# Optimization experiments

Hardware: AMD Instinct MI355X
Metric: run time of the kernel (lower is better)

The kernel has to match this reference:

```python
import jax, jax.numpy as jnp
import numpy as np

N_GENE = 100000
N_DIS = 20000
H = 128
E = 500000


def setup_inputs() -> dict:
    key = jax.random.key(0)
    ks = jax.random.split(key, 12)
    s1 = 1.0 / np.sqrt(2 * H)  # fan-in init scale, Linear(2H, H)
    s2 = 1.0 / np.sqrt(H)      # fan-in init scale, Linear(H, 1)
    z_gene = jax.random.normal(ks[0], (N_GENE, H), jnp.float32)
    z_disease = jax.random.normal(ks[1], (N_DIS, H), jnp.float32)
    # gene->disease edges: row indexes genes, col indexes diseases
    edges_gd = jnp.stack([
        jax.random.randint(ks[2], (E,), 0, N_GENE),
        jax.random.randint(ks[3], (E,), 0, N_DIS),
    ])
    # gene->gene edges
    edges_gg = jnp.stack([
        jax.random.randint(ks[4], (E,), 0, N_GENE),
        jax.random.randint(ks[5], (E,), 0, N_GENE),
    ])
    return {
        "z_gene": z_gene,
        "z_disease": z_disease,
        "edges_gd": edges_gd,
        "edges_gg": edges_gg,
        "w1_gd": jax.random.normal(ks[6], (2 * H, H), jnp.float32) * s1,
        "b1_gd": jnp.zeros((H,), jnp.float32),
        "w2_gd": jax.random.normal(ks[7], (H, 1), jnp.float32) * s2,
        "b2_gd": jnp.zeros((1,), jnp.float32),
        "w1_gg": jax.random.normal(ks[8], (2 * H, H), jnp.float32) * s1,
        "b1_gg": jnp.zeros((H,), jnp.float32),
        "w2_gg": jax.random.normal(ks[9], (H, 1), jnp.float32) * s2,
        "b2_gg": jnp.zeros((1,), jnp.float32),
    }


def _decode(z_src, z_dst, edges, w1, b1, w2, b2):
    # gather src/dst node embeddings by edge index, concat -> [E, 2H]
    z = jnp.concatenate([z_src[edges[0]], z_dst[edges[1]]], axis=1)
    h = jnp.maximum(z @ w1 + b1, 0.0)  # Linear + ReLU
    return h @ w2 + b2                  # Linear -> [E, 1]


def reference(z_gene, z_disease, edges_gd, edges_gg,
              w1_gd, b1_gd, w2_gd, b2_gd,
              w1_gg, b1_gg, w2_gg, b2_gg):
    out_gd = _decode(z_gene, z_disease, edges_gd, w1_gd, b1_gd, w2_gd, b2_gd)
    out_gg = _decode(z_gene, z_gene, edges_gg, w1_gg, b1_gg, w2_gg, b2_gg)
    # dict of per-relation outputs in the original; stack since E matches
    return jnp.stack([out_gd, out_gg])  # [2, E, 1]
```

## Files before the change

### kernel.cpp

```cpp
#include <hip/hip_runtime.h>
#include <hip/hip_bf16.h>

#define HDIM 128

typedef __attribute__((ext_vector_type(8))) short short8;
typedef __attribute__((ext_vector_type(4))) float floatx4;

__device__ __forceinline__ float bf2f(unsigned short u) {
    return __uint_as_float(((unsigned)u) << 16);
}
__device__ __forceinline__ unsigned short f2b(float f) {
    __hip_bfloat16 h = __float2bfloat16(f);
    return __builtin_bit_cast(unsigned short, h);
}
__device__ __forceinline__ float ldv(const void* p, size_t i, int flag) {
    return flag ? bf2f(((const unsigned short*)p)[i]) : ((const float*)p)[i];
}
__device__ __forceinline__ short8 pack8(float4 a, float4 b) {
    short8 r;
    r[0] = (short)f2b(a.x); r[1] = (short)f2b(a.y);
    r[2] = (short)f2b(a.z); r[3] = (short)f2b(a.w);
    r[4] = (short)f2b(b.x); r[5] = (short)f2b(b.y);
    r[6] = (short)f2b(b.z); r[7] = (short)f2b(b.w);
    return r;
}

__global__ __launch_bounds__(256) void detect_kernel(
    const unsigned short* __restrict__ zbits, int* __restrict__ flag)
{
    __shared__ int red[256];
    int tid = threadIdx.x;
    int cnt = 0;
    for (int i = tid; i < 4096; i += 256) {
        int ex = (zbits[i] >> 7) & 0xFF;
        if (ex >= 100 && ex <= 140) cnt++;
    }
    red[tid] = cnt;
    __syncthreads();
    for (int s = 128; s > 0; s >>= 1) {
        if (tid < s) red[tid] += red[tid + s];
        __syncthreads();
    }
    if (tid == 0) *flag = (red[0] >= 3686) ? 1 : 0;
}

__global__ __launch_bounds__(256) void wprep_kernel(
    const void* __restrict__ w1_gd, const void* __restrict__ w1_gg,
    const void* __restrict__ b1_gd, const void* __restrict__ w2_gd,
    const void* __restrict__ b2_gd, const void* __restrict__ b1_gg,
    const void* __restrict__ w2_gg, const void* __restrict__ b2_gg,
    unsigned short* __restrict__ img, float* __restrict__ params,
    const int* __restrict__ flagp)
{
    int b = blockIdx.x;
    int flag = *flagp;
    if (b < 4) {
        const void* w1 = (b < 2) ? w1_gd : w1_gg;
        int part = b & 1;
        unsigned short* out = img + b * 16384;
        for (int idx = threadIdx.x; idx < 16384; idx += 256) {
            int n   = idx >> 7;
            int rem = idx & 127;
            int g   = (rem >> 3) ^ (n & 15);
            int j   = rem & 7;
            size_t s = (size_t)(part * 128 + g * 8 + j) * 128 + n;
            out[idx] = flag ? ((const unsigned short*)w1)[s]
                            : f2b(((const float*)w1)[s]);
        }
    } else {
        int t = threadIdx.x;
        if (t < 128) {
            params[t]       = ldv(b1_gd, t, flag);
            params[256 + t] = ldv(b1_gg, t, flag);
        } else {
            params[t]       = ldv(w2_gd, t - 128, flag);
            params[256 + t] = ldv(w2_gg, t - 128, flag);
        }
        if (t == 0) {
            params[512] = ldv(b2_gd, 0, flag);
            params[513] = ldv(b2_gg, 0, flag);
        }
    }
}

__device__ __forceinline__ void load_zfrags(
    const void* Z, int r0c, int r1c, int quad, int flag, short8 zf[2][4])
{
    if (flag) {
        const uint4* z0 = (const uint4*)Z + (size_t)r0c * 16;
        const uint4* z1 = (const uint4*)Z + (size_t)r1c * 16;
#pragma unroll
        for (int kc = 0; kc < 4; ++kc) {
            zf[0][kc] = __builtin_bit_cast(short8, z0[kc * 4 + quad]);
            zf[1][kc] = __builtin_bit_cast(short8, z1[kc * 4 + quad]);
        }
    } else {
        const float4* z0 = (const float4*)Z + (size_t)r0c * 32;
        const float4* z1 = (const float4*)Z + (size_t)r1c * 32;
#pragma unroll
        for (int kc = 0; kc < 4; ++kc) {
            int o = kc * 8 + quad * 2;
            zf[0][kc] = pack8(z0[o], z0[o + 1]);
            zf[1][kc] = pack8(z1[o], z1[o + 1]);
        }
    }
}

__device__ __forceinline__ void mfma_pass_store(
    const uint4* sW, const short8 zf[2][4], int nl, int quad,
    int row0, int row1, int M, unsigned short* __restrict__ Out)
{
    floatx4 acc[2][8];
#pragma unroll
    for (int rt = 0; rt < 2; ++rt)
#pragma unroll
        for (int nt = 0; nt < 8; ++nt)
            acc[rt][nt] = (floatx4){0.f, 0.f, 0.f, 0.f};

#pragma unroll
    for (int kc = 0; kc < 4; ++kc) {
        int p = (kc * 4 + quad) ^ nl;
#pragma unroll
        for (int nt = 0; nt < 8; ++nt) {
            short8 wf = __builtin_bit_cast(short8, sW[(nt * 16 + nl) * 16 + p]);
            acc[0][nt] = __builtin_amdgcn_mfma_f32_16x16x32_bf16(wf, zf[0][kc], acc[0][nt], 0, 0, 0);
            acc[1][nt] = __builtin_amdgcn_mfma_f32_16x16x32_bf16(wf, zf[1][kc], acc[1][nt], 0, 0, 0);
        }
    }
#pragma unroll
    for (int rt = 0; rt < 2; ++rt) {
        int row = rt ? row1 : row0;
        if (row < M) {
#pragma unroll
            for (int nt = 0; nt < 8; ++nt) {
                ushort4 v;
                v.x = f2b(acc[rt][nt][0]);
                v.y = f2b(acc[rt][nt][1]);
                v.z = f2b(acc[rt][nt][2]);
                v.w = f2b(acc[rt][nt][3]);
                *(ushort4*)(Out + (size_t)row * HDIM + nt * 16 + quad * 4) = v;
            }
        }
    }
}

__global__ __launch_bounds__(256) void proj_gene3_kernel(
    const void* __restrict__ Z, const uint4* __restrict__ Wimg,
    unsigned short* __restrict__ A_gd, unsigned short* __restrict__ A_gg,
    unsigned short* __restrict__ B_gg, int M, const int* __restrict__ flagp)
{
    __shared__ uint4 sW[2048];
    int tid  = threadIdx.x;
    int lane = tid & 63;
    int wave = tid >> 6;
    int nl   = lane & 15;
    int quad = lane >> 4;

    int row0 = blockIdx.x * 128 + wave * 32 + nl;
    int row1 = row0 + 16;
    int r0c = row0 < M ? row0 : (M - 1);
    int r1c = row1 < M ? row1 : (M - 1);

    short8 zf[2][4];
    load_zfrags(Z, r0c, r1c, quad, *flagp, zf);

    const uint4* imgs[3] = {Wimg, Wimg + 2 * 2048, Wimg + 3 * 2048};
    unsigned short* outs[3] = {A_gd, A_gg, B_gg};
#pragma unroll
    for (int ph = 0; ph < 3; ++ph) {
        __syncthreads();
        const uint4* im = imgs[ph];
#pragma unroll
        for (int i = 0; i < 8; ++i) sW[tid + i * 256] = im[tid + i * 256];
        __syncthreads();
        mfma_pass_store(sW, zf, nl, quad, row0, row1, M, outs[ph]);
    }
}

__global__ __launch_bounds__(256) void proj1_kernel(
    const void* __restrict__ Z, const uint4* __restrict__ Wimg,
    unsigned short* __restrict__ Out, int M, const int* __restrict__ flagp)
{
    __shared__ uint4 sW[2048];
    int tid  = threadIdx.x;
    int lane = tid & 63;
    int wave = tid >> 6;
    int nl   = lane & 15;
    int quad = lane >> 4;

    int row0 = blockIdx.x * 128 + wave * 32 + nl;
    int row1 = row0 + 16;
    int r0c = row0 < M ? row0 : (M - 1);
    int r1c = row1 < M ? row1 : (M - 1);

    short8 zf[2][4];
    load_zfrags(Z, r0c, r1c, quad, *flagp, zf);

#pragma unroll
    for (int i = 0; i < 8; ++i) sW[tid + i * 256] = Wimg[tid + i * 256];
    __syncthreads();
    mfma_pass_store(sW, zf, nl, quad, row0, row1, M, Out);
}

__global__ __launch_bounds__(256) void edge_kernel(
    const int* __restrict__ edges_gd, const int* __restrict__ edges_gg,
    const unsigned short* __restrict__ A_gd, const unsigned short* __restrict__ B_gd,
    const unsigned short* __restrict__ A_gg, const unsigned short* __restrict__ B_gg,
    const float* __restrict__ params,
    void* __restrict__ out, int E, int eblk, const int* __restrict__ flagp)
{
    int rel = (blockIdx.x >= eblk) ? 1 : 0;
    int blk = blockIdx.x - rel * eblk;
    const int* edges = rel ? edges_gg : edges_gd;
    const unsigned short* A = rel ? A_gg : A_gd;
    const unsigned short* B = rel ? B_gg : B_gd;
    const float* pp = params + rel * 256;
    float b2f = params[512 + rel];
    size_t eoff = rel ? (size_t)E : 0;

    int tid  = threadIdx.x;
    int lane = tid & 63;
    int wave = tid >> 6;
    int nl   = lane & 7;
    int grp  = lane >> 3;

    float b1f[16], w2f[16];
#pragma unroll
    for (int i = 0; i < 4; ++i) {
        float4 tb = *(const float4*)(pp + nl * 16 + i * 4);
        float4 tw = *(const float4*)(pp + 128 + nl * 16 + i * 4);
        b1f[i * 4 + 0] = tb.x; b1f[i * 4 + 1] = tb.y;
        b1f[i * 4 + 2] = tb.z; b1f[i * 4 + 3] = tb.w;
        w2f[i * 4 + 0] = tw.x; w2f[i * 4 + 1] = tw.y;
        w2f[i * 4 + 2] = tw.z; w2f[i * 4 + 3] = tw.w;
    }

    int e = blk * 32 + wave * 8 + grp;
    float acc = 0.f;
    if (e < E) {
        int src = edges[e];
        int dst = edges[E + e];
        const uint4* ap = (const uint4*)(A + (size_t)src * HDIM) + nl * 2;
        const uint4* bp = (const uint4*)(B + (size_t)dst * HDIM) + nl * 2;
        uint4 a0 = ap[0], a1 = ap[1];
        uint4 c0 = bp[0], c1 = bp[1];
        const unsigned* au0 = (const unsigned*)&a0;
        const unsigned* au1 = (const unsigned*)&a1;
        const unsigned* cu0 = (const unsigned*)&c0;
        const unsigned* cu1 = (const unsigned*)&c1;
#pragma unroll
        for (int i = 0; i < 4; ++i) {
            float x0 = __uint_as_float(au0[i] << 16);
            float x1 = __uint_as_float(au0[i] & 0xffff0000u);
            float y0 = __uint_as_float(cu0[i] << 16);
            float y1 = __uint_as_float(cu0[i] & 0xffff0000u);
            float h0 = fmaxf(x0 + y0 + b1f[2 * i], 0.f);
            float h1 = fmaxf(x1 + y1 + b1f[2 * i + 1], 0.f);
            acc = fmaf(h0, w2f[2 * i], acc);
            acc = fmaf(h1, w2f[2 * i + 1], acc);
        }
#pragma unroll
        for (int i = 0; i < 4; ++i) {
            float x0 = __uint_as_float(au1[i] << 16);
            float x1 = __uint_as_float(au1[i] & 0xffff0000u);
            float y0 = __uint_as_float(cu1[i] << 16);
            float y1 = __uint_as_float(cu1[i] & 0xffff0000u);
            float h0 = fmaxf(x0 + y0 + b1f[8 + 2 * i], 0.f);
            float h1 = fmaxf(x1 + y1 + b1f[8 + 2 * i + 1], 0.f);
            acc = fmaf(h0, w2f[8 + 2 * i], acc);
            acc = fmaf(h1, w2f[8 + 2 * i + 1], acc);
        }
    }
    acc += __shfl_xor(acc, 1);
    acc += __shfl_xor(acc, 2);
    acc += __shfl_xor(acc, 4);
    if (e < E && nl == 0) {
        float r = acc + b2f;
        if (*flagp) ((unsigned short*)out)[eoff + e] = f2b(r);
        else        ((float*)out)[eoff + e] = r;
    }
}

__global__ __launch_bounds__(128) void naive_edge_kernel(
    const int* __restrict__ edges,
    const void* __restrict__ zsrc, const void* __restrict__ zdst,
    const void* __restrict__ w1, const void* __restrict__ b1,
    const void* __restrict__ w2, const void* __restrict__ b2,
    void* __restrict__ out, size_t eoff, int E,
    const int* __restrict__ flagp)
{
    int flag = flagp ? *flagp : 0;
    __shared__ float zs[128], zd[128], red[128];
    int e = blockIdx.x;
    int n = threadIdx.x;
    int src = edges[e], dst = edges[E + e];
    zs[n] = ldv(zsrc, (size_t)src * HDIM + n, flag);
    zd[n] = ldv(zdst, (size_t)dst * HDIM + n, flag);
    __syncthreads();
    float acc = ldv(b1, n, flag);
    for (int k = 0; k < 128; ++k) acc = fmaf(zs[k], ldv(w1, (size_t)k * HDIM + n, flag), acc);
    for (int k = 0; k < 128; ++k) acc = fmaf(zd[k], ldv(w1, (size_t)(128 + k) * HDIM + n, flag), acc);
    red[n] = fmaxf(acc, 0.f) * ldv(w2, n, flag);
    __syncthreads();
    for (int s = 64; s > 0; s >>= 1) {
        if (n < s) red[n] += red[n + s];
        __syncthreads();
    }
    if (n == 0) {
        float r = red[0] + ldv(b2, 0, flag);
        if (flag) ((unsigned short*)out)[eoff + e] = f2b(r);
        else      ((float*)out)[eoff + e] = r;
    }
}

extern "C" void kernel_launch(void* const* d_in, const int* in_sizes, int n_in,
                              void* d_out, int out_size, void* d_ws, size_t ws_size,
                              hipStream_t stream)
{
    const void* z_gene = d_in[0];
    const void* z_dis  = d_in[1];
    const int* edges_gd = (const int*)d_in[2];
    const int* edges_gg = (const int*)d_in[3];
    const void* w1_gd = d_in[4];
    const void* b1_gd = d_in[5];
    const void* w2_gd = d_in[6];
    const void* b2_gd = d_in[7];
    const void* w1_gg = d_in[8];
    const void* b1_gg = d_in[9];
    const void* w2_gg = d_in[10];
    const void* b2_gg = d_in[11];

    int NG = in_sizes[0] / HDIM;
    int ND = in_sizes[1] / HDIM;
    int E  = in_sizes[2] / 2;

    size_t off_flag   = 0;
    size_t off_params = 256;
    size_t off_img    = 2560;
    size_t off_Agd    = off_img + 131072;
    size_t off_Bgd    = off_Agd + (size_t)NG * HDIM * 2;
    size_t off_Agg    = off_Bgd + (size_t)ND * HDIM * 2;
    size_t off_Bgg    = off_Agg + (size_t)NG * HDIM * 2;
    size_t need       = off_Bgg + (size_t)NG * HDIM * 2;

    char* ws = (char*)d_ws;

    if (ws_size < need) {
        const int* flagp = nullptr;
        if (ws_size >= 16) {
            detect_kernel<<<1, 256, 0, stream>>>((const unsigned short*)z_gene, (int*)ws);
            flagp = (const int*)ws;
        }
        naive_edge_kernel<<<E, 128, 0, stream>>>(edges_gd, z_gene, z_dis,
                                                 w1_gd, b1_gd, w2_gd, b2_gd,
                                                 d_out, 0, E, flagp);
        naive_edge_kernel<<<E, 128, 0, stream>>>(edges_gg, z_gene, z_gene,
                                                 w1_gg, b1_gg, w2_gg, b2_gg,
                                                 d_out, (size_t)E, E, flagp);
        return;
    }

    int* flag = (int*)(ws + off_flag);
    float* params = (float*)(ws + off_params);
    unsigned short* img = (unsigned short*)(ws + off_img);
    unsigned short* Agd = (unsigned short*)(ws + off_Agd);
    unsigned short* Bgd = (unsigned short*)(ws + off_Bgd);
    unsigned short* Agg = (unsigned short*)(ws + off_Agg);
    unsigned short* Bgg = (unsigned short*)(ws + off_Bgg);

    detect_kernel<<<1, 256, 0, stream>>>((const unsigned short*)z_gene, flag);

    wprep_kernel<<<5, 256, 0, stream>>>(w1_gd, w1_gg, b1_gd, w2_gd, b2_gd,
                                        b1_gg, w2_gg, b2_gg, img, params, flag);

    const uint4* img4 = (const uint4*)img;
    int gblk = (NG + 127) / 128;
    int dblk = (ND + 127) / 128;
    proj_gene3_kernel<<<gblk, 256, 0, stream>>>(z_gene, img4, Agd, Agg, Bgg, NG, flag);
    proj1_kernel<<<dblk, 256, 0, stream>>>(z_dis, img4 + 2048, Bgd, ND, flag);

    int eblk = (E + 31) / 32;
    edge_kernel<<<2 * eblk, 256, 0, stream>>>(edges_gd, edges_gg, Agd, Bgd, Agg, Bgg,
                                              params, d_out, E, eblk, flag);
}
```

Before: 251.9 us.

## Fuse prep and projection kernels, fold bias into projection, thread-per-edge decode

```diff
diff --git a/kernel.cpp b/kernel.cpp
--- a/kernel.cpp
+++ b/kernel.cpp
@@ -25,9 +25,7 @@
     return r;
 }
 
-__global__ __launch_bounds__(256) void detect_kernel(
-    const unsigned short* __restrict__ zbits, int* __restrict__ flag)
-{
+__device__ __forceinline__ int local_detect(const unsigned short* zbits) {
     __shared__ int red[256];
     int tid = threadIdx.x;
     int cnt = 0;
@@ -41,19 +39,20 @@
         if (tid < s) red[tid] += red[tid + s];
         __syncthreads();
     }
-    if (tid == 0) *flag = (red[0] >= 3686) ? 1 : 0;
-}
-
-__global__ __launch_bounds__(256) void wprep_kernel(
+    return (red[0] >= 3686) ? 1 : 0;
+}
+
+__global__ __launch_bounds__(256) void prep_kernel(
+    const unsigned short* __restrict__ zbits,
     const void* __restrict__ w1_gd, const void* __restrict__ w1_gg,
     const void* __restrict__ b1_gd, const void* __restrict__ w2_gd,
     const void* __restrict__ b2_gd, const void* __restrict__ b1_gg,
     const void* __restrict__ w2_gg, const void* __restrict__ b2_gg,
     unsigned short* __restrict__ img, float* __restrict__ params,
-    const int* __restrict__ flagp)
-{
+    int* __restrict__ flagout)
+{
+    int flag = local_detect(zbits);
     int b = blockIdx.x;
-    int flag = *flagp;
     if (b < 4) {
         const void* w1 = (b < 2) ? w1_gd : w1_gg;
         int part = b & 1;
@@ -79,75 +78,17 @@
         if (t == 0) {
             params[512] = ldv(b2_gd, 0, flag);
             params[513] = ldv(b2_gg, 0, flag);
-        }
-    }
-}
-
-__device__ __forceinline__ void load_zfrags(
-    const void* Z, int r0c, int r1c, int quad, int flag, short8 zf[2][4])
-{
-    if (flag) {
-        const uint4* z0 = (const uint4*)Z + (size_t)r0c * 16;
-        const uint4* z1 = (const uint4*)Z + (size_t)r1c * 16;
-#pragma unroll
-        for (int kc = 0; kc < 4; ++kc) {
-            zf[0][kc] = __builtin_bit_cast(short8, z0[kc * 4 + quad]);
-            zf[1][kc] = __builtin_bit_cast(short8, z1[kc * 4 + quad]);
-        }
-    } else {
-        const float4* z0 = (const float4*)Z + (size_t)r0c * 32;
-        const float4* z1 = (const float4*)Z + (size_t)r1c * 32;
-#pragma unroll
-        for (int kc = 0; kc < 4; ++kc) {
-            int o = kc * 8 + quad * 2;
-            zf[0][kc] = pack8(z0[o], z0[o + 1]);
-            zf[1][kc] = pack8(z1[o], z1[o + 1]);
-        }
-    }
-}
-
-__device__ __forceinline__ void mfma_pass_store(
-    const uint4* sW, const short8 zf[2][4], int nl, int quad,
-    int row0, int row1, int M, unsigned short* __restrict__ Out)
-{
-    floatx4 acc[2][8];
-#pragma unroll
-    for (int rt = 0; rt < 2; ++rt)
-#pragma unroll
-        for (int nt = 0; nt < 8; ++nt)
-            acc[rt][nt] = (floatx4){0.f, 0.f, 0.f, 0.f};
-
-#pragma unroll
-    for (int kc = 0; kc < 4; ++kc) {
-        int p = (kc * 4 + quad) ^ nl;
-#pragma unroll
-        for (int nt = 0; nt < 8; ++nt) {
-            short8 wf = __builtin_bit_cast(short8, sW[(nt * 16 + nl) * 16 + p]);
-            acc[0][nt] = __builtin_amdgcn_mfma_f32_16x16x32_bf16(wf, zf[0][kc], acc[0][nt], 0, 0, 0);
-            acc[1][nt] = __builtin_amdgcn_mfma_f32_16x16x32_bf16(wf, zf[1][kc], acc[1][nt], 0, 0, 0);
-        }
-    }
-#pragma unroll
-    for (int rt = 0; rt < 2; ++rt) {
-        int row = rt ? row1 : row0;
-        if (row < M) {
-#pragma unroll
-            for (int nt = 0; nt < 8; ++nt) {
-                ushort4 v;
-                v.x = f2b(acc[rt][nt][0]);
-                v.y = f2b(acc[rt][nt][1]);
-                v.z = f2b(acc[rt][nt][2]);
-                v.w = f2b(acc[rt][nt][3]);
-                *(ushort4*)(Out + (size_t)row * HDIM + nt * 16 + quad * 4) = v;
-            }
-        }
-    }
-}
-
-__global__ __launch_bounds__(256) void proj_gene3_kernel(
-    const void* __restrict__ Z, const uint4* __restrict__ Wimg,
-    unsigned short* __restrict__ A_gd, unsigned short* __restrict__ A_gg,
-    unsigned short* __restrict__ B_gg, int M, const int* __restrict__ flagp)
+            *flagout = flag;
+        }
+    }
+}
+
+__global__ __launch_bounds__(256) void proj_all_kernel(
+    const void* __restrict__ Zg, const void* __restrict__ Zd,
+    const uint4* __restrict__ Wimg, const float* __restrict__ params,
+    unsigned short* __restrict__ A_gd, unsigned short* __restrict__ B_gd,
+    unsigned short* __restrict__ A_gg, unsigned short* __restrict__ B_gg,
+    int NG, int ND, int gblk, const int* __restrict__ flagp)
 {
     __shared__ uint4 sW[2048];
     int tid  = threadIdx.x;
@@ -155,51 +96,74 @@
     int wave = tid >> 6;
     int nl   = lane & 15;
     int quad = lane >> 4;
-
-    int row0 = blockIdx.x * 128 + wave * 32 + nl;
-    int row1 = row0 + 16;
-    int r0c = row0 < M ? row0 : (M - 1);
-    int r1c = row1 < M ? row1 : (M - 1);
-
-    short8 zf[2][4];
-    load_zfrags(Z, r0c, r1c, quad, *flagp, zf);
-
-    const uint4* imgs[3] = {Wimg, Wimg + 2 * 2048, Wimg + 3 * 2048};
-    unsigned short* outs[3] = {A_gd, A_gg, B_gg};
-#pragma unroll
-    for (int ph = 0; ph < 3; ++ph) {
+    int flag = *flagp;
+
+    bool gene = (int)blockIdx.x < gblk;
+    int blk = gene ? blockIdx.x : blockIdx.x - gblk;
+    int M = gene ? NG : ND;
+    const void* Z = gene ? Zg : Zd;
+
+    int row = blk * 64 + wave * 16 + nl;
+    int rc = row < M ? row : (M - 1);
+
+    short8 zf[4];
+    if (flag) {
+        const uint4* z = (const uint4*)Z + (size_t)rc * 16;
+#pragma unroll
+        for (int kc = 0; kc < 4; ++kc)
+            zf[kc] = __builtin_bit_cast(short8, z[kc * 4 + quad]);
+    } else {
+        const float4* z = (const float4*)Z + (size_t)rc * 32;
+#pragma unroll
+        for (int kc = 0; kc < 4; ++kc) {
+            int o = kc * 8 + quad * 2;
+            zf[kc] = pack8(z[o], z[o + 1]);
+        }
+    }
+
+    int nph = gene ? 3 : 1;
+    for (int ph = 0; ph < nph; ++ph) {
+        const uint4* im;
+        unsigned short* Out;
+        const float* bias;
+        if (gene) {
+            im   = Wimg + (ph == 0 ? 0 : ph == 1 ? 2 : 3) * 2048;
+            Out  = ph == 0 ? A_gd : ph == 1 ? A_gg : B_gg;
+            bias = ph == 0 ? params : ph == 1 ? params + 256 : nullptr;
+        } else {
+            im = Wimg + 2048; Out = B_gd; bias = nullptr;
+        }
         __syncthreads();
-        const uint4* im = imgs[ph];
 #pragma unroll
         for (int i = 0; i < 8; ++i) sW[tid + i * 256] = im[tid + i * 256];
         __syncthreads();
-        mfma_pass_store(sW, zf, nl, quad, row0, row1, M, outs[ph]);
-    }
-}
-
-__global__ __launch_bounds__(256) void proj1_kernel(
-    const void* __restrict__ Z, const uint4* __restrict__ Wimg,
-    unsigned short* __restrict__ Out, int M, const int* __restrict__ flagp)
-{
-    __shared__ uint4 sW[2048];
-    int tid  = threadIdx.x;
-    int lane = tid & 63;
-    int wave = tid >> 6;
-    int nl   = lane & 15;
-    int quad = lane >> 4;
-
-    int row0 = blockIdx.x * 128 + wave * 32 + nl;
-    int row1 = row0 + 16;
-    int r0c = row0 < M ? row0 : (M - 1);
-    int r1c = row1 < M ? row1 : (M - 1);
-
-    short8 zf[2][4];
-    load_zfrags(Z, r0c, r1c, quad, *flagp, zf);
-
-#pragma unroll
-    for (int i = 0; i < 8; ++i) sW[tid + i * 256] = Wimg[tid + i * 256];
-    __syncthreads();
-    mfma_pass_store(sW, zf, nl, quad, row0, row1, M, Out);
+
+        floatx4 acc[8];
+#pragma unroll
+        for (int nt = 0; nt < 8; ++nt) acc[nt] = (floatx4){0.f, 0.f, 0.f, 0.f};
+#pragma unroll
+        for (int kc = 0; kc < 4; ++kc) {
+            int p = (kc * 4 + quad) ^ nl;
+#pragma unroll
+            for (int nt = 0; nt < 8; ++nt) {
+                short8 wf = __builtin_bit_cast(short8, sW[(nt * 16 + nl) * 16 + p]);
+                acc[nt] = __builtin_amdgcn_mfma_f32_16x16x32_bf16(wf, zf[kc], acc[nt], 0, 0, 0);
+            }
+        }
+        if (row < M) {
+#pragma unroll
+            for (int nt = 0; nt < 8; ++nt) {
+                float4 bv = {0.f, 0.f, 0.f, 0.f};
+                if (bias) bv = *(const float4*)(bias + nt * 16 + quad * 4);
+                ushort4 v;
+                v.x = f2b(acc[nt][0] + bv.x);
+                v.y = f2b(acc[nt][1] + bv.y);
+                v.z = f2b(acc[nt][2] + bv.z);
+                v.w = f2b(acc[nt][3] + bv.w);
+                *(ushort4*)(Out + (size_t)row * HDIM + nt * 16 + quad * 4) = v;
+            }
+        }
+    }
 }
 
 __global__ __launch_bounds__(256) void edge_kernel(
@@ -207,78 +171,58 @@
     const unsigned short* __restrict__ A_gd, const unsigned short* __restrict__ B_gd,
     const unsigned short* __restrict__ A_gg, const unsigned short* __restrict__ B_gg,
     const float* __restrict__ params,
-    void* __restrict__ out, int E, int eblk, const int* __restrict__ flagp)
-{
-    int rel = (blockIdx.x >= eblk) ? 1 : 0;
-    int blk = blockIdx.x - rel * eblk;
+    void* __restrict__ out, int E, int nb, const int* __restrict__ flagp)
+{
+    int rel = ((int)blockIdx.x >= nb) ? 1 : 0;
+    int e = (blockIdx.x - rel * nb) * 256 + threadIdx.x;
+    if (e >= E) return;
+
     const int* edges = rel ? edges_gg : edges_gd;
     const unsigned short* A = rel ? A_gg : A_gd;
     const unsigned short* B = rel ? B_gg : B_gd;
-    const float* pp = params + rel * 256;
-    float b2f = params[512 + rel];
-    size_t eoff = rel ? (size_t)E : 0;
-
-    int tid  = threadIdx.x;
-    int lane = tid & 63;
-    int wave = tid >> 6;
-    int nl   = lane & 7;
-    int grp  = lane >> 3;
-
-    float b1f[16], w2f[16];
-#pragma unroll
-    for (int i = 0; i < 4; ++i) {
-        float4 tb = *(const float4*)(pp + nl * 16 + i * 4);
-        float4 tw = *(const float4*)(pp + 128 + nl * 16 + i * 4);
-        b1f[i * 4 + 0] = tb.x; b1f[i * 4 + 1] = tb.y;
-        b1f[i * 4 + 2] = tb.z; b1f[i * 4 + 3] = tb.w;
-        w2f[i * 4 + 0] = tw.x; w2f[i * 4 + 1] = tw.y;
-        w2f[i * 4 + 2] = tw.z; w2f[i * 4 + 3] = tw.w;
-    }
-
-    int e = blk * 32 + wave * 8 + grp;
+    const float* w2 = params + 128 + rel * 256;
+    float b2 = params[512 + rel];
+
+    int src = edges[e];
+    int dst = edges[E + e];
+    const uint4* ar = (const uint4*)(A + (size_t)src * HDIM);
+    const uint4* br = (const uint4*)(B + (size_t)dst * HDIM);
+
     float acc = 0.f;
-    if (e < E) {
-        int src = edges[e];
-        int dst = edges[E + e];
-        const uint4* ap = (const uint4*)(A + (size_t)src * HDIM) + nl * 2;
-        const uint4* bp = (const uint4*)(B + (size_t)dst * HDIM) + nl * 2;
-        uint4 a0 = ap[0], a1 = ap[1];
-        uint4 c0 = bp[0], c1 = bp[1];
-        const unsigned* au0 = (const unsigned*)&a0;
-        const unsigned* au1 = (const unsigned*)&a1;
-        const unsigned* cu0 = (const unsigned*)&c0;
-        const unsigned* cu1 = (const unsigned*)&c1;
+#pragma unroll
+    for (int g = 0; g < 4; ++g) {
+        uint4 a[4], b[4];
+#pragma unroll
+        for (int i = 0; i < 4; ++i) { a[i] = ar[g * 4 + i]; b[i] = br[g * 4 + i]; }
 #pragma unroll
         for (int i = 0; i < 4; ++i) {
-            float x0 = __uint_as_float(au0[i] << 16);
-            float x1 = __uint_as_float(au0[i] & 0xffff0000u);
-            float y0 = __uint_as_float(cu0[i] << 16);
-            float y1 = __uint_as_float(cu0[i] & 0xffff0000u);
-            float h0 = fmaxf(x0 + y0 + b1f[2 * i], 0.f);
-            float h1 = fmaxf(x1 + y1 + b1f[2 * i + 1], 0.f);
-            acc = fmaf(h0, w2f[2 * i], acc);
-            acc = fmaf(h1, w2f[2 * i + 1], acc);
-        }
-#pragma unroll
-        for (int i = 0; i < 4; ++i) {
-            float x0 = __uint_as_float(au1[i] << 16);
-            float x1 = __uint_as_float(au1[i] & 0xffff0000u);
-            float y0 = __uint_as_float(cu1[i] << 16);
-            float y1 = __uint_as_float(cu1[i] & 0xffff0000u);
-            float h0 = fmaxf(x0 + y0 + b1f[8 + 2 * i], 0.f);
-            float h1 = fmaxf(x1 + y1 + b1f[8 + 2 * i + 1], 0.f);
-            acc = fmaf(h0, w2f[8 + 2 * i], acc);
-            acc = fmaf(h1, w2f[8 + 2 * i + 1], acc);
-        }
-    }
-    acc += __shfl_xor(acc, 1);
-    acc += __shfl_xor(acc, 2);
-    acc += __shfl_xor(acc, 4);
-    if (e < E && nl == 0) {
-        float r = acc + b2f;
-        if (*flagp) ((unsigned short*)out)[eoff + e] = f2b(r);
-        else        ((float*)out)[eoff + e] = r;
-    }
+            const unsigned* au = (const unsigned*)&a[i];
+            const unsigned* bu = (const unsigned*)&b[i];
+#pragma unroll
+            for (int j = 0; j < 4; ++j) {
+                int ch = g * 32 + i * 8 + j * 2;
+                float x0 = __uint_as_float(au[j] << 16);
+                float x1 = __uint_as_float(au[j] & 0xffff0000u);
+                float y0 = __uint_as_float(bu[j] << 16);
+                float y1 = __uint_as_float(bu[j] & 0xffff0000u);
+                float h0 = fmaxf(x0 + y0, 0.f);
+                float h1 = fmaxf(x1 + y1, 0.f);
+                acc = fmaf(h0, w2[ch], acc);
+                acc = fmaf(h1, w2[ch + 1], acc);
+            }
+        }
+    }
+    float r = acc + b2;
+    size_t o = (size_t)rel * E + e;
+    if (*flagp) ((unsigned short*)out)[o] = f2b(r);
+    else        ((float*)out)[o] = r;
+}
+
+__global__ __launch_bounds__(256) void detect_kernel(
+    const unsigned short* __restrict__ zbits, int* __restrict__ flag)
+{
+    int f = local_detect(zbits);
+    if (threadIdx.x == 0) *flag = f;
 }
 
 __global__ __launch_bounds__(128) void naive_edge_kernel(
@@ -368,18 +312,18 @@
     unsigned short* Agg = (unsigned short*)(ws + off_Agg);
     unsigned short* Bgg = (unsigned short*)(ws + off_Bgg);
 
-    detect_kernel<<<1, 256, 0, stream>>>((const unsigned short*)z_gene, flag);
-
-    wprep_kernel<<<5, 256, 0, stream>>>(w1_gd, w1_gg, b1_gd, w2_gd, b2_gd,
-                                        b1_gg, w2_gg, b2_gg, img, params, flag);
+    prep_kernel<<<5, 256, 0, stream>>>((const unsigned short*)z_gene,
+                                       w1_gd, w1_gg, b1_gd, w2_gd, b2_gd,
+                                       b1_gg, w2_gg, b2_gg, img, params, flag);
 
     const uint4* img4 = (const uint4*)img;
-    int gblk = (NG + 127) / 128;
-    int dblk = (ND + 127) / 128;
-    proj_gene3_kernel<<<gblk, 256, 0, stream>>>(z_gene, img4, Agd, Agg, Bgg, NG, flag);
-    proj1_kernel<<<dblk, 256, 0, stream>>>(z_dis, img4 + 2048, Bgd, ND, flag);
-
-    int eblk = (E + 31) / 32;
-    edge_kernel<<<2 * eblk, 256, 0, stream>>>(edges_gd, edges_gg, Agd, Bgd, Agg, Bgg,
-                                              params, d_out, E, eblk, flag);
-}
+    int gblk = (NG + 63) / 64;
+    int dblk = (ND + 63) / 64;
+    proj_all_kernel<<<gblk + dblk, 256, 0, stream>>>(z_gene, z_dis, img4, params,
+                                                     Agd, Bgd, Agg, Bgg,
+                                                     NG, ND, gblk, flag);
+
+    int nb = (E + 255) / 256;
+    edge_kernel<<<2 * nb, 256, 0, stream>>>(edges_gd, edges_gg, Agd, Bgd, Agg, Bgg,
+                                            params, d_out, E, nb, flag);
+}
```

Result: slower. 262.1 us (+4.1%).
